# Performance work log

Hardware: AMD Instinct MI355X
Metric: run time of the kernel (lower is better)

## Reference

```python
import jax, jax.numpy as jnp
import numpy as np

# ---- hash-grid config (from module source) ----
L = 16          # n_levels
F = 2           # n_features_per_level
T = 1 << 19     # hashmap size
BASE = 16
SCALE = 1.3819
RES = [int(np.floor(BASE * SCALE ** l)) for l in range(L)]
DENSE = [(r + 1) ** 3 <= T for r in RES]   # levels 0-4 dense, rest hashed
PRIMES = np.array([1, 2654435761, 805459861], dtype=np.uint32)
OFFS = np.array([[i, j, k] for k in (0, 1) for j in (0, 1) for i in (0, 1)], dtype=np.float32)  # [8,3]
OFFS_U = OFFS.astype(np.uint32)


def hash_grid_encode(xyz, table):
    # xyz: [N,3] in [0,1); table: [L,T,F]
    feats = []
    for l in range(L):
        res = RES[l]
        pos = xyz * res                      # [N,3]
        p0f = jnp.floor(pos)
        w = pos - p0f                        # trilinear weights, [N,3]
        p0 = p0f.astype(jnp.uint32)          # [N,3]
        corner = p0[:, None, :] + OFFS_U[None]            # [N,8,3] uint32
        if DENSE[l]:
            s = np.uint32(res + 1)
            idx = corner[..., 0] + corner[..., 1] * s + corner[..., 2] * (s * s)
        else:
            idx = (corner[..., 0] * PRIMES[0]) ^ (corner[..., 1] * PRIMES[1]) ^ (corner[..., 2] * PRIMES[2])
            idx = idx % np.uint32(T)
        # corner weights: prod_d (offs ? w : 1-w)  -> [N,8]
        wts = jnp.prod(jnp.where(OFFS[None].astype(bool), w[:, None, :], 1.0 - w[:, None, :]), axis=-1)
        f = table[l][idx]                    # gather: [N,8,F]
        feats.append(jnp.sum(f * wts[..., None], axis=1))  # [N,F]
    return jnp.concatenate(feats, axis=-1)   # [N, L*F=32]


def sh_deg4(d):
    # d in [-1,1]^3; returns [N,16] real SH basis (tcnn ordering/constants)
    x, y, z = d[:, 0], d[:, 1], d[:, 2]
    x2, y2, z2 = x * x, y * y, z * z
    xy, yz, xz = x * y, y * z, x * z
    return jnp.stack([
        jnp.full_like(x, 0.28209479177387814),
        -0.48860251190291987 * y,
        0.48860251190291987 * z,
        -0.48860251190291987 * x,
        1.0925484305920792 * xy,
        -1.0925484305920792 * yz,
        0.94617469575755997 * z2 - 0.31539156525251999,
        -1.0925484305920792 * xz,
        0.54627421529603959 * (x2 - y2),
        0.59004358992664352 * y * (-3.0 * x2 + y2),
        2.8906114426405538 * xy * z,
        0.45704579946446572 * y * (1.0 - 5.0 * z2),
        0.3731763325901154 * z * (5.0 * z2 - 3.0),
        0.45704579946446572 * x * (1.0 - 5.0 * z2),
        1.4453057213202769 * z * (x2 - y2),
        0.59004358992664352 * x * (-x2 + 3.0 * y2),
    ], axis=-1)


def setup_inputs() -> dict:
    key = jax.random.key(0)
    ks = jax.random.split(key, 8)
    N = 2 ** 21
    xyz = jax.random.uniform(ks[0], (N, 3), dtype=jnp.float32)
    dir = jax.random.uniform(ks[1], (N, 3), dtype=jnp.float32)
    # hash table init per tcnn: uniform in [-1e-4, 1e-4]
    hash_table = jax.random.uniform(ks[2], (L, T, F), dtype=jnp.float32, minval=-1e-4, maxval=1e-4)
    def he(k, fan_in, shape):
        return jax.random.normal(k, shape, dtype=jnp.float32) * np.sqrt(2.0 / fan_in)
    w_sigma1 = he(ks[3], 32, (32, 64))
    w_sigma2 = he(ks[4], 64, (64, 17))   # 1 + geo_feat_dim(16)
    w_rgb1 = he(ks[5], 32, (32, 64))     # 16 (SH) + 16 (geo)
    w_rgb2 = he(ks[6], 64, (64, 64))
    w_rgb3 = he(ks[7], 64, (64, 3))
    return {"xyz": xyz, "dir": dir, "hash_table": hash_table,
            "w_sigma1": w_sigma1, "w_sigma2": w_sigma2,
            "w_rgb1": w_rgb1, "w_rgb2": w_rgb2, "w_rgb3": w_rgb3}


def reference(xyz, dir, hash_table, w_sigma1, w_sigma2, w_rgb1, w_rgb2, w_rgb3):
    xyz_flat = xyz.reshape(-1, 3)
    dir_flat = dir.reshape(-1, 3)
    enc = hash_grid_encode(xyz_flat, hash_table)                 # [N,32]
    h = jax.nn.relu(enc @ w_sigma1)
    geometry = h @ w_sigma2                                       # [N,17]
    sigma, geo_feat = geometry[..., :1], geometry[..., 1:]
    dir_enc = sh_deg4(dir_flat * 2.0 - 1.0)                       # [N,16]
    rgb_in = jnp.concatenate([dir_enc, geo_feat], axis=-1)        # [N,32]
    h = jax.nn.relu(rgb_in @ w_rgb1)
    h = jax.nn.relu(h @ w_rgb2)
    rgb = h @ w_rgb3                                              # [N,3]
    rgb_unflat = rgb.reshape(xyz.shape)
    sigma_unflat = sigma.reshape(xyz.shape[:-1] + (1,))
    return jax.nn.sigmoid(rgb_unflat), jax.nn.relu(sigma_unflat)
```

## Files before the change

kernel.cpp:

```cpp
#include <hip/hip_runtime.h>
#include <hip/hip_bf16.h>
#include <cmath>

#define TBL (1 << 19)

__device__ __forceinline__ float relu_f(float x) { return fmaxf(x, 0.0f); }

__device__ __forceinline__ unsigned short f2bf(float x) {
    union { float f; unsigned u; } v; v.f = x;
    const unsigned r = v.u + 0x7FFFu + ((v.u >> 16) & 1u);
    return (unsigned short)(r >> 16);
}

typedef __attribute__((ext_vector_type(8))) short short8;
typedef __attribute__((ext_vector_type(4))) float floatx4;

#define RES_LIST {16, 22, 30, 42, 58, 80, 111, 153, 212, 294, 406, 561, 775, 1072, 1481, 2047}

__global__ __launch_bounds__(256, 8)
void encode_pinned(const float* __restrict__ xyz,
                   const float* __restrict__ table,
                   float* __restrict__ ws_enc,
                   unsigned levels_packed,
                   int n)
{
    constexpr unsigned RES[16] = RES_LIST;

    const unsigned sub = blockIdx.x & 7u;
    const unsigned level = (levels_packed >> (4u * sub)) & 0xFu;
    const int i = (int)(blockIdx.x >> 3) * 256 + (int)threadIdx.x;
    if (i >= n) return;

    const float px_ = __builtin_nontemporal_load(xyz + 3 * (size_t)i + 0);
    const float py_ = __builtin_nontemporal_load(xyz + 3 * (size_t)i + 1);
    const float pz_ = __builtin_nontemporal_load(xyz + 3 * (size_t)i + 2);

    const unsigned res = RES[level];
    const float fr = (float)res;
    const float posx = px_ * fr, posy = py_ * fr, posz = pz_ * fr;
    const float fx = floorf(posx), fy = floorf(posy), fz = floorf(posz);
    const float wx = posx - fx, wy = posy - fy, wz = posz - fz;
    const unsigned x0 = (unsigned)fx, y0 = (unsigned)fy, z0 = (unsigned)fz;
    const float* tb = table + (size_t)level * (TBL * 2);

    float a0 = 0.0f, a1 = 0.0f;
    if (level < 5) {
        const unsigned s = res + 1u;
        const unsigned s2 = s * s;
#pragma unroll
        for (int c = 0; c < 8; ++c) {
            const unsigned cx = x0 + (c & 1);
            const unsigned cy = y0 + ((c >> 1) & 1);
            const unsigned cz = z0 + ((c >> 2) & 1);
            const unsigned idx = cx + cy * s + cz * s2;
            const float w = ((c & 1) ? wx : 1.0f - wx) *
                            ((c & 2) ? wy : 1.0f - wy) *
                            ((c & 4) ? wz : 1.0f - wz);
            const float2 f = *reinterpret_cast<const float2*>(tb + 2u * idx);
            a0 = fmaf(f.x, w, a0);
            a1 = fmaf(f.y, w, a1);
        }
    } else {
#pragma unroll
        for (int c = 0; c < 8; ++c) {
            const unsigned cx = x0 + (c & 1);
            const unsigned cy = y0 + ((c >> 1) & 1);
            const unsigned cz = z0 + ((c >> 2) & 1);
            unsigned idx = (cx * 1u) ^ (cy * 2654435761u) ^ (cz * 805459861u);
            idx &= (unsigned)(TBL - 1);
            const float w = ((c & 1) ? wx : 1.0f - wx) *
                            ((c & 2) ? wy : 1.0f - wy) *
                            ((c & 4) ? wz : 1.0f - wz);
            const float2 f = *reinterpret_cast<const float2*>(tb + 2u * idx);
            a0 = fmaf(f.x, w, a0);
            a1 = fmaf(f.y, w, a1);
        }
    }

    float* dst = ws_enc + 2 * ((size_t)level * n + i);
    __builtin_nontemporal_store(a0, dst + 0);
    __builtin_nontemporal_store(a1, dst + 1);
}

__global__ __launch_bounds__(256)
void mlp_mfma(const float* __restrict__ ws_enc,
              const float* __restrict__ dirv,
              const float* __restrict__ ws1,
              const float* __restrict__ ws2,
              const float* __restrict__ wr1,
              const float* __restrict__ wr2,
              const float* __restrict__ wr3,
              float* __restrict__ out,
              int n)
{
    __shared__ alignas(16) unsigned short s_w[13184];
    __shared__ alignas(16) unsigned short s_act[4 * 16 * 72];
    __shared__ alignas(16) float          s_geo[4 * 16 * 20];

    const int tid = threadIdx.x;

    for (int e = tid; e < 13184; e += 256) s_w[e] = 0;
    __syncthreads();
    for (int e = tid; e < 2048; e += 256) { const int k = e >> 6, j = e & 63; s_w[0     + j * 40 + k] = f2bf(ws1[e]); }
    for (int e = tid; e < 1088; e += 256) { const int k = e / 17, j = e % 17; s_w[2560  + j * 72 + k] = f2bf(ws2[e]); }
    for (int e = tid; e < 2048; e += 256) { const int k = e >> 6, j = e & 63; s_w[4864  + j * 40 + k] = f2bf(wr1[e]); }
    for (int e = tid; e < 4096; e += 256) { const int k = e >> 6, j = e & 63; s_w[7424  + j * 72 + k] = f2bf(wr2[e]); }
    for (int e = tid; e < 192;  e += 256) { const int k = e / 3,  j = e % 3;  s_w[12032 + j * 72 + k] = f2bf(wr3[e]); }
    __syncthreads();

    const int wave = tid >> 6;
    const int lane = tid & 63;
    const int q    = lane >> 4;
    const int mr   = lane & 15;
    unsigned short* hb = s_act + wave * (16 * 72);
    float*          gb = s_geo + wave * (16 * 20);
    const int base = blockIdx.x * 256 + wave * 64;
    if (base >= n) return;

#pragma unroll 1
    for (int mt = 0; mt < 4; ++mt) {
        const int pt = base + mt * 16 + mr;

        short8 aenc;
#pragma unroll
        for (int t = 0; t < 4; ++t) {
            const float2 e = *reinterpret_cast<const float2*>(ws_enc + 2 * ((size_t)(q * 4 + t) * n + pt));
            aenc[2 * t + 0] = (short)f2bf(e.x);
            aenc[2 * t + 1] = (short)f2bf(e.y);
        }

#pragma unroll
        for (int nc = 0; nc < 4; ++nc) {
            const short8 b = *reinterpret_cast<const short8*>(s_w + 0 + (nc * 16 + mr) * 40 + q * 8);
            floatx4 acc = {0.f, 0.f, 0.f, 0.f};
            acc = __builtin_amdgcn_mfma_f32_16x16x32_bf16(aenc, b, acc, 0, 0, 0);
#pragma unroll
            for (int r = 0; r < 4; ++r)
                hb[(q * 4 + r) * 72 + nc * 16 + mr] = f2bf(fmaxf(acc[r], 0.f));
        }
        __builtin_amdgcn_wave_barrier();

        {
            const short8 a0 = *reinterpret_cast<const short8*>(hb + mr * 72 + 0  + q * 8);
            const short8 a1 = *reinterpret_cast<const short8*>(hb + mr * 72 + 32 + q * 8);
            floatx4 acc0 = {0.f, 0.f, 0.f, 0.f};
            floatx4 acc1 = {0.f, 0.f, 0.f, 0.f};
            {
                const short8 b0 = *reinterpret_cast<const short8*>(s_w + 2560 + mr * 72 + 0  + q * 8);
                const short8 b1 = *reinterpret_cast<const short8*>(s_w + 2560 + mr * 72 + 32 + q * 8);
                acc0 = __builtin_amdgcn_mfma_f32_16x16x32_bf16(a0, b0, acc0, 0, 0, 0);
                acc0 = __builtin_amdgcn_mfma_f32_16x16x32_bf16(a1, b1, acc0, 0, 0, 0);
            }
            {
                const short8 b0 = *reinterpret_cast<const short8*>(s_w + 2560 + (16 + mr) * 72 + 0  + q * 8);
                const short8 b1 = *reinterpret_cast<const short8*>(s_w + 2560 + (16 + mr) * 72 + 32 + q * 8);
                acc1 = __builtin_amdgcn_mfma_f32_16x16x32_bf16(a0, b0, acc1, 0, 0, 0);
                acc1 = __builtin_amdgcn_mfma_f32_16x16x32_bf16(a1, b1, acc1, 0, 0, 0);
            }
#pragma unroll
            for (int r = 0; r < 4; ++r) gb[(q * 4 + r) * 20 + mr + 3] = acc0[r];
            if (mr == 0) {
#pragma unroll
                for (int r = 0; r < 4; ++r) gb[(q * 4 + r) * 20 + 19] = acc1[r];
            }
        }
        __builtin_amdgcn_wave_barrier();

        if (lane < 16)
            out[3 * (size_t)n + (size_t)(base + mt * 16 + lane)] = fmaxf(gb[lane * 20 + 3], 0.f);

        const float dx = dirv[3 * (size_t)pt + 0] * 2.0f - 1.0f;
        const float dy = dirv[3 * (size_t)pt + 1] * 2.0f - 1.0f;
        const float dz = dirv[3 * (size_t)pt + 2] * 2.0f - 1.0f;
        const float x2 = dx * dx, y2 = dy * dy, z2 = dz * dz;
        const float xy = dx * dy, yz = dy * dz, xz = dx * dz;
        float sh[16];
        sh[0]  = 0.28209479177387814f;
        sh[1]  = -0.48860251190291987f * dy;
        sh[2]  = 0.48860251190291987f * dz;
        sh[3]  = -0.48860251190291987f * dx;
        sh[4]  = 1.0925484305920792f * xy;
        sh[5]  = -1.0925484305920792f * yz;
        sh[6]  = 0.94617469575756f * z2 - 0.31539156525252f;
        sh[7]  = -1.0925484305920792f * xz;
        sh[8]  = 0.5462742152960396f * (x2 - y2);
        sh[9]  = 0.5900435899266435f * dy * (-3.0f * x2 + y2);
        sh[10] = 2.890611442640554f * xy * dz;
        sh[11] = 0.4570457994644657f * dy * (1.0f - 5.0f * z2);
        sh[12] = 0.3731763325901154f * dz * (5.0f * z2 - 3.0f);
        sh[13] = 0.4570457994644657f * dx * (1.0f - 5.0f * z2);
        sh[14] = 1.445305721320277f * dz * (x2 - y2);
        sh[15] = 0.5900435899266435f * dx * (-x2 + 3.0f * y2);

        short8 ar;
        if (q < 2) {
#pragma unroll
            for (int j = 0; j < 8; ++j) ar[j] = (short)f2bf(sh[q * 8 + j]);
        } else {
            const floatx4 g0 = *reinterpret_cast<const floatx4*>(gb + mr * 20 + 4 + (q - 2) * 8);
            const floatx4 g1 = *reinterpret_cast<const floatx4*>(gb + mr * 20 + 8 + (q - 2) * 8);
#pragma unroll
            for (int j = 0; j < 4; ++j) { ar[j] = (short)f2bf(g0[j]); ar[4 + j] = (short)f2bf(g1[j]); }
        }

#pragma unroll
        for (int nc = 0; nc < 4; ++nc) {
            const short8 b = *reinterpret_cast<const short8*>(s_w + 4864 + (nc * 16 + mr) * 40 + q * 8);
            floatx4 acc = {0.f, 0.f, 0.f, 0.f};
            acc = __builtin_amdgcn_mfma_f32_16x16x32_bf16(ar, b, acc, 0, 0, 0);
#pragma unroll
            for (int r = 0; r < 4; ++r)
                hb[(q * 4 + r) * 72 + nc * 16 + mr] = f2bf(fmaxf(acc[r], 0.f));
        }
        __builtin_amdgcn_wave_barrier();

        {
            const short8 a0 = *reinterpret_cast<const short8*>(hb + mr * 72 + 0  + q * 8);
            const short8 a1 = *reinterpret_cast<const short8*>(hb + mr * 72 + 32 + q * 8);
            __builtin_amdgcn_wave_barrier();
#pragma unroll
            for (int nc = 0; nc < 4; ++nc) {
                const short8 b0 = *reinterpret_cast<const short8*>(s_w + 7424 + (nc * 16 + mr) * 72 + 0  + q * 8);
                const short8 b1 = *reinterpret_cast<const short8*>(s_w + 7424 + (nc * 16 + mr) * 72 + 32 + q * 8);
                floatx4 acc = {0.f, 0.f, 0.f, 0.f};
                acc = __builtin_amdgcn_mfma_f32_16x16x32_bf16(a0, b0, acc, 0, 0, 0);
                acc = __builtin_amdgcn_mfma_f32_16x16x32_bf16(a1, b1, acc, 0, 0, 0);
#pragma unroll
                for (int r = 0; r < 4; ++r)
                    hb[(q * 4 + r) * 72 + nc * 16 + mr] = f2bf(fmaxf(acc[r], 0.f));
            }
        }
        __builtin_amdgcn_wave_barrier();

        {
            const short8 a0 = *reinterpret_cast<const short8*>(hb + mr * 72 + 0  + q * 8);
            const short8 a1 = *reinterpret_cast<const short8*>(hb + mr * 72 + 32 + q * 8);
            const short8 b0 = *reinterpret_cast<const short8*>(s_w + 12032 + mr * 72 + 0  + q * 8);
            const short8 b1 = *reinterpret_cast<const short8*>(s_w + 12032 + mr * 72 + 32 + q * 8);
            floatx4 acc = {0.f, 0.f, 0.f, 0.f};
            acc = __builtin_amdgcn_mfma_f32_16x16x32_bf16(a0, b0, acc, 0, 0, 0);
            acc = __builtin_amdgcn_mfma_f32_16x16x32_bf16(a1, b1, acc, 0, 0, 0);
            if (mr < 3) {
#pragma unroll
                for (int r = 0; r < 4; ++r) {
                    const int p = base + mt * 16 + q * 4 + r;
                    out[3 * (size_t)p + mr] = 1.0f / (1.0f + __expf(-acc[r]));
                }
            }
        }
        __builtin_amdgcn_wave_barrier();
    }
}

__global__ __launch_bounds__(256, 4)
void nerf_fused(const float* __restrict__ xyz,
                const float* __restrict__ dirv,
                const float* __restrict__ table,
                const float* __restrict__ ws1,
                const float* __restrict__ ws2,
                const float* __restrict__ wr1,
                const float* __restrict__ wr2,
                const float* __restrict__ wr3,
                float* __restrict__ out,
                int n)
{
    constexpr unsigned RES[16] = RES_LIST;

    const int i = blockIdx.x * 256 + threadIdx.x;
    if (i >= n) return;

    const float px_ = xyz[3 * (size_t)i + 0];
    const float py_ = xyz[3 * (size_t)i + 1];
    const float pz_ = xyz[3 * (size_t)i + 2];

    float enc[32];
#pragma unroll
    for (int l = 0; l < 16; ++l) {
        const unsigned res = RES[l];
        const float fr = (float)res;
        const float posx = px_ * fr, posy = py_ * fr, posz = pz_ * fr;
        const float fx = floorf(posx), fy = floorf(posy), fz = floorf(posz);
        const float wx = posx - fx, wy = posy - fy, wz = posz - fz;
        const unsigned x0 = (unsigned)fx, y0 = (unsigned)fy, z0 = (unsigned)fz;
        const float* tb = table + (size_t)l * (TBL * 2);
        float a0 = 0.0f, a1 = 0.0f;
#pragma unroll
        for (int c = 0; c < 8; ++c) {
            const unsigned cx = x0 + (c & 1);
            const unsigned cy = y0 + ((c >> 1) & 1);
            const unsigned cz = z0 + ((c >> 2) & 1);
            unsigned idx;
            if (l < 5) {
                const unsigned s = res + 1u;
                idx = cx + cy * s + cz * (s * s);
            } else {
                idx = (cx * 1u) ^ (cy * 2654435761u) ^ (cz * 805459861u);
                idx &= (unsigned)(TBL - 1);
            }
            const float w = ((c & 1) ? wx : 1.0f - wx) *
                            ((c & 2) ? wy : 1.0f - wy) *
                            ((c & 4) ? wz : 1.0f - wz);
            const float2 f = *reinterpret_cast<const float2*>(tb + 2u * idx);
            a0 = fmaf(f.x, w, a0);
            a1 = fmaf(f.y, w, a1);
        }
        enc[2 * l + 0] = a0;
        enc[2 * l + 1] = a1;
    }

    float h[64];
#pragma unroll
    for (int j = 0; j < 64; ++j) h[j] = 0.0f;
#pragma unroll
    for (int k = 0; k < 32; ++k) {
        const float e = enc[k];
#pragma unroll
        for (int j = 0; j < 64; ++j) h[j] = fmaf(e, ws1[k * 64 + j], h[j]);
    }
#pragma unroll
    for (int j = 0; j < 64; ++j) h[j] = relu_f(h[j]);

    float geo[17];
#pragma unroll
    for (int j = 0; j < 17; ++j) geo[j] = 0.0f;
#pragma unroll
    for (int k = 0; k < 64; ++k) {
        const float e = h[k];
#pragma unroll
        for (int j = 0; j < 17; ++j) geo[j] = fmaf(e, ws2[k * 17 + j], geo[j]);
    }
    out[3 * (size_t)n + (size_t)i] = relu_f(geo[0]);

    const float dx = dirv[3 * (size_t)i + 0] * 2.0f - 1.0f;
    const float dy = dirv[3 * (size_t)i + 1] * 2.0f - 1.0f;
    const float dz = dirv[3 * (size_t)i + 2] * 2.0f - 1.0f;
    const float x2 = dx * dx, y2 = dy * dy, z2 = dz * dz;
    const float xy = dx * dy, yz = dy * dz, xz = dx * dz;

    float sh[16];
    sh[0]  = 0.28209479177387814f;
    sh[1]  = -0.48860251190291987f * dy;
    sh[2]  = 0.48860251190291987f * dz;
    sh[3]  = -0.48860251190291987f * dx;
    sh[4]  = 1.0925484305920792f * xy;
    sh[5]  = -1.0925484305920792f * yz;
    sh[6]  = 0.94617469575756f * z2 - 0.31539156525252f;
    sh[7]  = -1.0925484305920792f * xz;
    sh[8]  = 0.5462742152960396f * (x2 - y2);
    sh[9]  = 0.5900435899266435f * dy * (-3.0f * x2 + y2);
    sh[10] = 2.890611442640554f * xy * dz;
    sh[11] = 0.4570457994644657f * dy * (1.0f - 5.0f * z2);
    sh[12] = 0.3731763325901154f * dz * (5.0f * z2 - 3.0f);
    sh[13] = 0.4570457994644657f * dx * (1.0f - 5.0f * z2);
    sh[14] = 1.445305721320277f * dz * (x2 - y2);
    sh[15] = 0.5900435899266435f * dx * (-x2 + 3.0f * y2);

    float g[64];
#pragma unroll
    for (int j = 0; j < 64; ++j) g[j] = 0.0f;
#pragma unroll
    for (int k = 0; k < 16; ++k) {
        const float e = sh[k];
#pragma unroll
        for (int j = 0; j < 64; ++j) g[j] = fmaf(e, wr1[k * 64 + j], g[j]);
    }
#pragma unroll
    for (int k = 16; k < 32; ++k) {
        const float e = geo[k - 15];
#pragma unroll
        for (int j = 0; j < 64; ++j) g[j] = fmaf(e, wr1[k * 64 + j], g[j]);
    }
#pragma unroll
    for (int j = 0; j < 64; ++j) g[j] = relu_f(g[j]);

    float r0 = 0.0f, r1 = 0.0f, r2 = 0.0f;
#pragma unroll
    for (int half = 0; half < 2; ++half) {
        const int j0 = half * 32;
        float g2h[32];
#pragma unroll
        for (int j = 0; j < 32; ++j) g2h[j] = 0.0f;
#pragma unroll
        for (int k = 0; k < 64; ++k) {
            const float e = g[k];
#pragma unroll
            for (int j = 0; j < 32; ++j) g2h[j] = fmaf(e, wr2[k * 64 + j0 + j], g2h[j]);
        }
#pragma unroll
        for (int j = 0; j < 32; ++j) {
            const float e = relu_f(g2h[j]);
            r0 = fmaf(e, wr3[(j0 + j) * 3 + 0], r0);
            r1 = fmaf(e, wr3[(j0 + j) * 3 + 1], r1);
            r2 = fmaf(e, wr3[(j0 + j) * 3 + 2], r2);
        }
    }

    out[3 * (size_t)i + 0] = 1.0f / (1.0f + __expf(-r0));
    out[3 * (size_t)i + 1] = 1.0f / (1.0f + __expf(-r1));
    out[3 * (size_t)i + 2] = 1.0f / (1.0f + __expf(-r2));
}

extern "C" void kernel_launch(void* const* d_in, const int* in_sizes, int n_in,
                              void* d_out, int out_size, void* d_ws, size_t ws_size,
                              hipStream_t stream)
{
    const float* xyz   = (const float*)d_in[0];
    const float* dirv  = (const float*)d_in[1];
    const float* table = (const float*)d_in[2];
    const float* ws1   = (const float*)d_in[3];
    const float* ws2   = (const float*)d_in[4];
    const float* wr1   = (const float*)d_in[5];
    const float* wr2   = (const float*)d_in[6];
    const float* wr3   = (const float*)d_in[7];
    float* out = (float*)d_out;

    const int n = in_sizes[0] / 3;
    const int blocks_per_level = (n + 255) / 256;
    dim3 block(256);
    dim3 grid_mlp(blocks_per_level);
    dim3 grid_enc(8 * blocks_per_level);

    const size_t enc_bytes = (size_t)n * 16 * sizeof(float2);
    if (ws_size >= enc_bytes && (n & 255) == 0) {
        float* ws_enc = (float*)d_ws;
        hipLaunchKernelGGL(encode_pinned, grid_enc, block, 0, stream,
                           xyz, table, ws_enc, 0xCBA98765u, n);
        hipLaunchKernelGGL(encode_pinned, grid_enc, block, 0, stream,
                           xyz, table, ws_enc, 0x43210FEDu, n);
        hipLaunchKernelGGL(mlp_mfma, grid_mlp, block, 0, stream,
                           ws_enc, dirv, ws1, ws2, wr1, wr2, wr3, out, n);
    } else {
        hipLaunchKernelGGL(nerf_fused, grid_mlp, block, 0, stream,
                           xyz, dirv, table, ws1, ws2, wr1, wr2, wr3, out, n);
    }
}
```

Baseline: 1.108 ms.

## Pair x-adjacent corner gathers into float4 loads and batch MLP tiles

The encode kernel now processes the eight trilinear corners as four x-pairs. For each pair it issues one aligned float4 load that covers both corners when they share a 16-byte block, and falls back to a second float2 load otherwise. The aim is to cut the number of random gather transactions into the hash table. The MLP kernel processes two 16-point tiles per iteration with double-buffered shared activations, and stores the geometry features as bf16 instead of fp32. It also drops the early return on out-of-range blocks and issues the sigma output directly from registers. The batching adds ILP around the MFMA chains at the cost of more registers and shared memory.

New measurement: 1.294 ms. 16.8% more time.

```diff
diff --git a/kernel.cpp b/kernel.cpp
--- a/kernel.cpp
+++ b/kernel.cpp
@@ -42,39 +42,40 @@
     const float wx = posx - fx, wy = posy - fy, wz = posz - fz;
     const unsigned x0 = (unsigned)fx, y0 = (unsigned)fy, z0 = (unsigned)fz;
     const float* tb = table + (size_t)level * (TBL * 2);
+    const bool dense = (level < 5);
+    const unsigned s = res + 1u;
+    const unsigned s2 = s * s;
 
     float a0 = 0.0f, a1 = 0.0f;
-    if (level < 5) {
-        const unsigned s = res + 1u;
-        const unsigned s2 = s * s;
-#pragma unroll
-        for (int c = 0; c < 8; ++c) {
-            const unsigned cx = x0 + (c & 1);
-            const unsigned cy = y0 + ((c >> 1) & 1);
-            const unsigned cz = z0 + ((c >> 2) & 1);
-            const unsigned idx = cx + cy * s + cz * s2;
-            const float w = ((c & 1) ? wx : 1.0f - wx) *
-                            ((c & 2) ? wy : 1.0f - wy) *
-                            ((c & 4) ? wz : 1.0f - wz);
-            const float2 f = *reinterpret_cast<const float2*>(tb + 2u * idx);
-            a0 = fmaf(f.x, w, a0);
-            a1 = fmaf(f.y, w, a1);
-        }
-    } else {
-#pragma unroll
-        for (int c = 0; c < 8; ++c) {
-            const unsigned cx = x0 + (c & 1);
-            const unsigned cy = y0 + ((c >> 1) & 1);
-            const unsigned cz = z0 + ((c >> 2) & 1);
-            unsigned idx = (cx * 1u) ^ (cy * 2654435761u) ^ (cz * 805459861u);
-            idx &= (unsigned)(TBL - 1);
-            const float w = ((c & 1) ? wx : 1.0f - wx) *
-                            ((c & 2) ? wy : 1.0f - wy) *
-                            ((c & 4) ? wz : 1.0f - wz);
-            const float2 f = *reinterpret_cast<const float2*>(tb + 2u * idx);
-            a0 = fmaf(f.x, w, a0);
-            a1 = fmaf(f.y, w, a1);
-        }
+#pragma unroll
+    for (int p = 0; p < 4; ++p) {
+        const unsigned cy = y0 + (p & 1);
+        const unsigned cz = z0 + (p >> 1);
+        unsigned ia, ib;
+        if (dense) {
+            ia = x0 + cy * s + cz * s2;
+            ib = ia + 1u;
+        } else {
+            const unsigned h = (cy * 2654435761u) ^ (cz * 805459861u);
+            ia = (x0 ^ h) & (unsigned)(TBL - 1);
+            ib = ((x0 + 1u) ^ h) & (unsigned)(TBL - 1);
+        }
+        const float wyz = ((p & 1) ? wy : 1.0f - wy) * ((p & 2) ? wz : 1.0f - wz);
+        const float wa = (1.0f - wx) * wyz;
+        const float wb = wx * wyz;
+
+        const float4 blk = *reinterpret_cast<const float4*>(tb + 2u * (ia & ~1u));
+        const bool hi = (ia & 1u) != 0u;
+        const float fa0 = hi ? blk.z : blk.x;
+        const float fa1 = hi ? blk.w : blk.y;
+        float fb0 = hi ? blk.x : blk.z;
+        float fb1 = hi ? blk.y : blk.w;
+        if (ib != (ia ^ 1u)) {
+            const float2 fb = *reinterpret_cast<const float2*>(tb + 2u * ib);
+            fb0 = fb.x; fb1 = fb.y;
+        }
+        a0 = fmaf(fa0, wa, fmaf(fb0, wb, a0));
+        a1 = fmaf(fa1, wa, fmaf(fb1, wb, a1));
     }
 
     float* dst = ws_enc + 2 * ((size_t)level * n + i);
@@ -94,8 +95,8 @@
               int n)
 {
     __shared__ alignas(16) unsigned short s_w[13184];
-    __shared__ alignas(16) unsigned short s_act[4 * 16 * 72];
-    __shared__ alignas(16) float          s_geo[4 * 16 * 20];
+    __shared__ alignas(16) unsigned short s_act[4 * 2 * 16 * 72];
+    __shared__ alignas(16) unsigned short s_geo[4 * 2 * 16 * 16];
 
     const int tid = threadIdx.x;
 
@@ -112,129 +113,148 @@
     const int lane = tid & 63;
     const int q    = lane >> 4;
     const int mr   = lane & 15;
-    unsigned short* hb = s_act + wave * (16 * 72);
-    float*          gb = s_geo + wave * (16 * 20);
+    unsigned short* const hb0 = s_act + wave * (2 * 16 * 72);
+    unsigned short* const gb0 = s_geo + wave * (2 * 16 * 16);
     const int base = blockIdx.x * 256 + wave * 64;
-    if (base >= n) return;
 
 #pragma unroll 1
-    for (int mt = 0; mt < 4; ++mt) {
-        const int pt = base + mt * 16 + mr;
-
-        short8 aenc;
-#pragma unroll
-        for (int t = 0; t < 4; ++t) {
-            const float2 e = *reinterpret_cast<const float2*>(ws_enc + 2 * ((size_t)(q * 4 + t) * n + pt));
-            aenc[2 * t + 0] = (short)f2bf(e.x);
-            aenc[2 * t + 1] = (short)f2bf(e.y);
-        }
-
-#pragma unroll
-        for (int nc = 0; nc < 4; ++nc) {
-            const short8 b = *reinterpret_cast<const short8*>(s_w + 0 + (nc * 16 + mr) * 40 + q * 8);
-            floatx4 acc = {0.f, 0.f, 0.f, 0.f};
-            acc = __builtin_amdgcn_mfma_f32_16x16x32_bf16(aenc, b, acc, 0, 0, 0);
-#pragma unroll
-            for (int r = 0; r < 4; ++r)
-                hb[(q * 4 + r) * 72 + nc * 16 + mr] = f2bf(fmaxf(acc[r], 0.f));
-        }
-        __builtin_amdgcn_wave_barrier();
-
-        {
-            const short8 a0 = *reinterpret_cast<const short8*>(hb + mr * 72 + 0  + q * 8);
-            const short8 a1 = *reinterpret_cast<const short8*>(hb + mr * 72 + 32 + q * 8);
+    for (int bt = 0; bt < 2; ++bt) {
+        const int tb0 = base + bt * 32;
+
+        short8 aenc[2];
+#pragma unroll
+        for (int t = 0; t < 2; ++t) {
+            const int pt = tb0 + t * 16 + mr;
+#pragma unroll
+            for (int tt = 0; tt < 4; ++tt) {
+                const float2 e = *reinterpret_cast<const float2*>(
+                    ws_enc + 2 * ((size_t)(q * 4 + tt) * n + pt));
+                aenc[t][2 * tt + 0] = (short)f2bf(e.x);
+                aenc[t][2 * tt + 1] = (short)f2bf(e.y);
+            }
+        }
+
+#pragma unroll
+        for (int t = 0; t < 2; ++t) {
+            unsigned short* const hbt = hb0 + t * (16 * 72);
+#pragma unroll
+            for (int nc = 0; nc < 4; ++nc) {
+                const short8 b = *reinterpret_cast<const short8*>(s_w + (nc * 16 + mr) * 40 + q * 8);
+                floatx4 acc = {0.f, 0.f, 0.f, 0.f};
+                acc = __builtin_amdgcn_mfma_f32_16x16x32_bf16(aenc[t], b, acc, 0, 0, 0);
+#pragma unroll
+                for (int r = 0; r < 4; ++r)
+                    hbt[(q * 4 + r) * 72 + nc * 16 + mr] = f2bf(fmaxf(acc[r], 0.f));
+            }
+        }
+        __builtin_amdgcn_wave_barrier();
+
+#pragma unroll
+        for (int t = 0; t < 2; ++t) {
+            unsigned short* const hbt = hb0 + t * (16 * 72);
+            unsigned short* const gbt = gb0 + t * (16 * 16);
+            const short8 a0 = *reinterpret_cast<const short8*>(hbt + mr * 72 + 0  + q * 8);
+            const short8 a1 = *reinterpret_cast<const short8*>(hbt + mr * 72 + 32 + q * 8);
+            const short8 b00 = *reinterpret_cast<const short8*>(s_w + 2560 + mr * 72 + 0  + q * 8);
+            const short8 b01 = *reinterpret_cast<const short8*>(s_w + 2560 + mr * 72 + 32 + q * 8);
+            const short8 b10 = *reinterpret_cast<const short8*>(s_w + 2560 + (16 + mr) * 72 + 0  + q * 8);
+            const short8 b11 = *reinterpret_cast<const short8*>(s_w + 2560 + (16 + mr) * 72 + 32 + q * 8);
             floatx4 acc0 = {0.f, 0.f, 0.f, 0.f};
             floatx4 acc1 = {0.f, 0.f, 0.f, 0.f};
-            {
-                const short8 b0 = *reinterpret_cast<const short8*>(s_w + 2560 + mr * 72 + 0  + q * 8);
-                const short8 b1 = *reinterpret_cast<const short8*>(s_w + 2560 + mr * 72 + 32 + q * 8);
-                acc0 = __builtin_amdgcn_mfma_f32_16x16x32_bf16(a0, b0, acc0, 0, 0, 0);
-                acc0 = __builtin_amdgcn_mfma_f32_16x16x32_bf16(a1, b1, acc0, 0, 0, 0);
-            }
-            {
-                const short8 b0 = *reinterpret_cast<const short8*>(s_w + 2560 + (16 + mr) * 72 + 0  + q * 8);
-                const short8 b1 = *reinterpret_cast<const short8*>(s_w + 2560 + (16 + mr) * 72 + 32 + q * 8);
-                acc1 = __builtin_amdgcn_mfma_f32_16x16x32_bf16(a0, b0, acc1, 0, 0, 0);
-                acc1 = __builtin_amdgcn_mfma_f32_16x16x32_bf16(a1, b1, acc1, 0, 0, 0);
-            }
-#pragma unroll
-            for (int r = 0; r < 4; ++r) gb[(q * 4 + r) * 20 + mr + 3] = acc0[r];
+            acc0 = __builtin_amdgcn_mfma_f32_16x16x32_bf16(a0, b00, acc0, 0, 0, 0);
+            acc0 = __builtin_amdgcn_mfma_f32_16x16x32_bf16(a1, b01, acc0, 0, 0, 0);
+            acc1 = __builtin_amdgcn_mfma_f32_16x16x32_bf16(a0, b10, acc1, 0, 0, 0);
+            acc1 = __builtin_amdgcn_mfma_f32_16x16x32_bf16(a1, b11, acc1, 0, 0, 0);
             if (mr == 0) {
 #pragma unroll
-                for (int r = 0; r < 4; ++r) gb[(q * 4 + r) * 20 + 19] = acc1[r];
-            }
-        }
-        __builtin_amdgcn_wave_barrier();
-
-        if (lane < 16)
-            out[3 * (size_t)n + (size_t)(base + mt * 16 + lane)] = fmaxf(gb[lane * 20 + 3], 0.f);
-
-        const float dx = dirv[3 * (size_t)pt + 0] * 2.0f - 1.0f;
-        const float dy = dirv[3 * (size_t)pt + 1] * 2.0f - 1.0f;
-        const float dz = dirv[3 * (size_t)pt + 2] * 2.0f - 1.0f;
-        const float x2 = dx * dx, y2 = dy * dy, z2 = dz * dz;
-        const float xy = dx * dy, yz = dy * dz, xz = dx * dz;
-        float sh[16];
-        sh[0]  = 0.28209479177387814f;
-        sh[1]  = -0.48860251190291987f * dy;
-        sh[2]  = 0.48860251190291987f * dz;
-        sh[3]  = -0.48860251190291987f * dx;
-        sh[4]  = 1.0925484305920792f * xy;
-        sh[5]  = -1.0925484305920792f * yz;
-        sh[6]  = 0.94617469575756f * z2 - 0.31539156525252f;
-        sh[7]  = -1.0925484305920792f * xz;
-        sh[8]  = 0.5462742152960396f * (x2 - y2);
-        sh[9]  = 0.5900435899266435f * dy * (-3.0f * x2 + y2);
-        sh[10] = 2.890611442640554f * xy * dz;
-        sh[11] = 0.4570457994644657f * dy * (1.0f - 5.0f * z2);
-        sh[12] = 0.3731763325901154f * dz * (5.0f * z2 - 3.0f);
-        sh[13] = 0.4570457994644657f * dx * (1.0f - 5.0f * z2);
-        sh[14] = 1.445305721320277f * dz * (x2 - y2);
-        sh[15] = 0.5900435899266435f * dx * (-x2 + 3.0f * y2);
-
-        short8 ar;
-        if (q < 2) {
-#pragma unroll
-            for (int j = 0; j < 8; ++j) ar[j] = (short)f2bf(sh[q * 8 + j]);
-        } else {
-            const floatx4 g0 = *reinterpret_cast<const floatx4*>(gb + mr * 20 + 4 + (q - 2) * 8);
-            const floatx4 g1 = *reinterpret_cast<const floatx4*>(gb + mr * 20 + 8 + (q - 2) * 8);
-#pragma unroll
-            for (int j = 0; j < 4; ++j) { ar[j] = (short)f2bf(g0[j]); ar[4 + j] = (short)f2bf(g1[j]); }
-        }
-
-#pragma unroll
-        for (int nc = 0; nc < 4; ++nc) {
-            const short8 b = *reinterpret_cast<const short8*>(s_w + 4864 + (nc * 16 + mr) * 40 + q * 8);
-            floatx4 acc = {0.f, 0.f, 0.f, 0.f};
-            acc = __builtin_amdgcn_mfma_f32_16x16x32_bf16(ar, b, acc, 0, 0, 0);
-#pragma unroll
-            for (int r = 0; r < 4; ++r)
-                hb[(q * 4 + r) * 72 + nc * 16 + mr] = f2bf(fmaxf(acc[r], 0.f));
-        }
-        __builtin_amdgcn_wave_barrier();
-
-        {
-            const short8 a0 = *reinterpret_cast<const short8*>(hb + mr * 72 + 0  + q * 8);
-            const short8 a1 = *reinterpret_cast<const short8*>(hb + mr * 72 + 32 + q * 8);
-            __builtin_amdgcn_wave_barrier();
+                for (int r = 0; r < 4; ++r) {
+                    out[3 * (size_t)n + (size_t)(tb0 + t * 16 + q * 4 + r)] = fmaxf(acc0[r], 0.f);
+                    gbt[(q * 4 + r) * 16 + 15] = f2bf(acc1[r]);
+                }
+            } else {
+#pragma unroll
+                for (int r = 0; r < 4; ++r)
+                    gbt[(q * 4 + r) * 16 + (mr - 1)] = f2bf(acc0[r]);
+            }
+        }
+        __builtin_amdgcn_wave_barrier();
+
+#pragma unroll
+        for (int t = 0; t < 2; ++t) {
+            unsigned short* const hbt = hb0 + t * (16 * 72);
+            unsigned short* const gbt = gb0 + t * (16 * 16);
+            short8 ar;
+            if (q < 2) {
+                const int pt = tb0 + t * 16 + mr;
+                const float dx = dirv[3 * (size_t)pt + 0] * 2.0f - 1.0f;
+                const float dy = dirv[3 * (size_t)pt + 1] * 2.0f - 1.0f;
+                const float dz = dirv[3 * (size_t)pt + 2] * 2.0f - 1.0f;
+                const float x2 = dx * dx, y2 = dy * dy, z2 = dz * dz;
+                const float xy = dx * dy, yz = dy * dz, xz = dx * dz;
+                if (q == 0) {
+                    ar[0] = (short)f2bf(0.28209479177387814f);
+                    ar[1] = (short)f2bf(-0.48860251190291987f * dy);
+                    ar[2] = (short)f2bf(0.48860251190291987f * dz);
+                    ar[3] = (short)f2bf(-0.48860251190291987f * dx);
+                    ar[4] = (short)f2bf(1.0925484305920792f * xy);
+                    ar[5] = (short)f2bf(-1.0925484305920792f * yz);
+                    ar[6] = (short)f2bf(0.94617469575756f * z2 - 0.31539156525252f);
+                    ar[7] = (short)f2bf(-1.0925484305920792f * xz);
+                } else {
+                    ar[0] = (short)f2bf(0.5462742152960396f * (x2 - y2));
+                    ar[1] = (short)f2bf(0.5900435899266435f * dy * (-3.0f * x2 + y2));
+                    ar[2] = (short)f2bf(2.890611442640554f * xy * dz);
+                    ar[3] = (short)f2bf(0.4570457994644657f * dy * (1.0f - 5.0f * z2));
+                    ar[4] = (short)f2bf(0.3731763325901154f * dz * (5.0f * z2 - 3.0f));
+                    ar[5] = (short)f2bf(0.4570457994644657f * dx * (1.0f - 5.0f * z2));
+                    ar[6] = (short)f2bf(1.445305721320277f * dz * (x2 - y2));
+                    ar[7] = (short)f2bf(0.5900435899266435f * dx * (-x2 + 3.0f * y2));
+                }
+            } else {
+                ar = *reinterpret_cast<const short8*>(gbt + mr * 16 + (q - 2) * 8);
+            }
+#pragma unroll
+            for (int nc = 0; nc < 4; ++nc) {
+                const short8 b = *reinterpret_cast<const short8*>(s_w + 4864 + (nc * 16 + mr) * 40 + q * 8);
+                floatx4 acc = {0.f, 0.f, 0.f, 0.f};
+                acc = __builtin_amdgcn_mfma_f32_16x16x32_bf16(ar, b, acc, 0, 0, 0);
+#pragma unroll
+                for (int r = 0; r < 4; ++r)
+                    hbt[(q * 4 + r) * 72 + nc * 16 + mr] = f2bf(fmaxf(acc[r], 0.f));
+            }
+        }
+        __builtin_amdgcn_wave_barrier();
+
+        short8 ga[2][2];
+#pragma unroll
+        for (int t = 0; t < 2; ++t) {
+            unsigned short* const hbt = hb0 + t * (16 * 72);
+            ga[t][0] = *reinterpret_cast<const short8*>(hbt + mr * 72 + 0  + q * 8);
+            ga[t][1] = *reinterpret_cast<const short8*>(hbt + mr * 72 + 32 + q * 8);
+        }
+        __builtin_amdgcn_wave_barrier();
+#pragma unroll
+        for (int t = 0; t < 2; ++t) {
+            unsigned short* const hbt = hb0 + t * (16 * 72);
 #pragma unroll
             for (int nc = 0; nc < 4; ++nc) {
                 const short8 b0 = *reinterpret_cast<const short8*>(s_w + 7424 + (nc * 16 + mr) * 72 + 0  + q * 8);
                 const short8 b1 = *reinterpret_cast<const short8*>(s_w + 7424 + (nc * 16 + mr) * 72 + 32 + q * 8);
                 floatx4 acc = {0.f, 0.f, 0.f, 0.f};
-                acc = __builtin_amdgcn_mfma_f32_16x16x32_bf16(a0, b0, acc, 0, 0, 0);
-                acc = __builtin_amdgcn_mfma_f32_16x16x32_bf16(a1, b1, acc, 0, 0, 0);
+                acc = __builtin_amdgcn_mfma_f32_16x16x32_bf16(ga[t][0], b0, acc, 0, 0, 0);
+                acc = __builtin_amdgcn_mfma_f32_16x16x32_bf16(ga[t][1], b1, acc, 0, 0, 0);
 #pragma unroll
                 for (int r = 0; r < 4; ++r)
-                    hb[(q * 4 + r) * 72 + nc * 16 + mr] = f2bf(fmaxf(acc[r], 0.f));
-            }
-        }
-        __builtin_amdgcn_wave_barrier();
-
-        {
-            const short8 a0 = *reinterpret_cast<const short8*>(hb + mr * 72 + 0  + q * 8);
-            const short8 a1 = *reinterpret_cast<const short8*>(hb + mr * 72 + 32 + q * 8);
+                    hbt[(q * 4 + r) * 72 + nc * 16 + mr] = f2bf(fmaxf(acc[r], 0.f));
+            }
+        }
+        __builtin_amdgcn_wave_barrier();
+
+#pragma unroll
+        for (int t = 0; t < 2; ++t) {
+            unsigned short* const hbt = hb0 + t * (16 * 72);
+            const short8 a0 = *reinterpret_cast<const short8*>(hbt + mr * 72 + 0  + q * 8);
+            const short8 a1 = *reinterpret_cast<const short8*>(hbt + mr * 72 + 32 + q * 8);
             const short8 b0 = *reinterpret_cast<const short8*>(s_w + 12032 + mr * 72 + 0  + q * 8);
             const short8 b1 = *reinterpret_cast<const short8*>(s_w + 12032 + mr * 72 + 32 + q * 8);
             floatx4 acc = {0.f, 0.f, 0.f, 0.f};
@@ -243,7 +263,7 @@
             if (mr < 3) {
 #pragma unroll
                 for (int r = 0; r < 4; ++r) {
-                    const int p = base + mt * 16 + q * 4 + r;
+                    const int p = tb0 + t * 16 + q * 4 + r;
                     out[3 * (size_t)p + mr] = 1.0f / (1.0f + __expf(-acc[r]));
                 }
             }
```
